# Performance work log

Hardware: AMD Instinct MI355X
Metric: run time of the kernel (lower is better)

## Reference

```python
import jax, jax.numpy as jnp
import numpy as np
from jax import lax

HEADS = 8
LN_EPS = 1e-5


def setup_inputs() -> dict:
    key = jax.random.key(0)
    k = jax.random.split(key, 8)
    B, C, H, W, r = 4, 64, 64, 64, 4
    T = H * W
    x = jax.random.normal(k[0], (B, C, H, W), dtype=jnp.float32)
    conv_w = jax.random.normal(k[1], (C, C, r, r), dtype=jnp.float32) * 0.02  # OIHW
    conv_b = jnp.zeros((C,), dtype=jnp.float32)
    ln_g = jnp.ones((C,), dtype=jnp.float32)
    ln_b = jnp.zeros((C,), dtype=jnp.float32)
    Wqkv = jax.random.normal(k[2], (C, 3 * C), dtype=jnp.float32) * 0.02  # to_qvk (no bias)
    W0 = jax.random.normal(k[3], (C, C), dtype=jnp.float32) * 0.02  # output proj (no bias)
    E = jax.random.normal(k[4], (T, T // 4), dtype=jnp.float32)  # Linformer proj (randn in torch fwd)
    return {"x": x, "conv_w": conv_w, "conv_b": conv_b, "ln_g": ln_g,
            "ln_b": ln_b, "Wqkv": Wqkv, "W0": W0, "E": E}


def _layernorm2d(y, g, b):
    # LayerNorm over channel dim of NCHW (torch: permute to NHWC, LN last dim)
    yt = y.transpose(0, 2, 3, 1)  # b h w c
    mu = yt.mean(-1, keepdims=True)
    var = ((yt - mu) ** 2).mean(-1, keepdims=True)
    yt = (yt - mu) * lax.rsqrt(var + LN_EPS) * g + b
    return yt.transpose(0, 3, 1, 2)


def reference(x, conv_w, conv_b, ln_g, ln_b, Wqkv, W0, E):
    B, C, H, W = x.shape
    T = H * W
    dh = C // HEADS
    r = conv_w.shape[-1]

    # reducer: conv(stride=r) + LayerNorm2d. NOTE: faithful to the torch module,
    # this result is computed but NEVER used by the output (dead code in source).
    red = lax.conv_general_dilated(x, conv_w, (r, r), 'VALID',
                                   dimension_numbers=('NCHW', 'OIHW', 'NCHW'))
    red = red + conv_b[None, :, None, None]
    _red = _layernorm2d(red, ln_g, ln_b)  # unused, matches source

    # tokens from full-resolution x: b c h w -> b (h w) c
    xf = x.reshape(B, C, T).transpose(0, 2, 1)  # [B,T,C]
    qkv = xf @ Wqkv  # [B,T,3C]
    # rearrange 'b t (d k h)' with k=3, h=HEADS -> composite order (d, k, h)
    qkv = qkv.reshape(B, T, dh, 3, HEADS)
    q = qkv[:, :, :, 0, :].transpose(0, 3, 1, 2)  # [B,h,T,d]
    kk = qkv[:, :, :, 1, :].transpose(0, 3, 1, 2)
    v = qkv[:, :, :, 2, :].transpose(0, 3, 1, 2)

    # Linformer low-rank projection of V and K: [B,h,T,d] x [T,k] -> [B,h,k,d]
    v = jnp.einsum('bhjd,jk->bhkd', v, E)
    kk = jnp.einsum('bhjd,jk->bhkd', kk, E)

    scale = dh ** -0.5
    scores = jnp.einsum('bhid,bhjd->bhij', q, kk) * scale  # [B,h,T,k]
    attn = jax.nn.softmax(scores, axis=-1)
    out = jnp.einsum('bhij,bhjd->bhid', attn, v)  # [B,h,T,d]

    out = out.transpose(0, 2, 1, 3).reshape(B, T, C)  # b h i d -> b i (h d)
    out = out @ W0  # [B,T,C]
    return out.transpose(0, 2, 1).reshape(B, C, H, W)
```

## Files before the change

kernel.cpp:

```cpp
#include <hip/hip_runtime.h>

#define T_DIM 4096
#define KD    1024
#define SCALE2 (0.35355339059327373f * 1.4426950408889634f)
#define XS2_PITCH 520
#define XP_PITCH 17
#define WK_PITCH 136
#define VC_H 648

extern "C" __device__ float __ocml_native_exp2_f32(float);

typedef __attribute__((ext_vector_type(8))) short bf16x8;
typedef __attribute__((ext_vector_type(4))) float f32x4;
typedef __attribute__((ext_vector_type(16))) float f32x16;

__device__ inline unsigned short f2bf(float f) {
  unsigned u = __float_as_uint(f);
  unsigned r = u + 0x7fffu + ((u >> 16) & 1u);
  return (unsigned short)(r >> 16);
}

__device__ inline unsigned cvt_pk_bf16(float a, float b) {
  unsigned ua = __float_as_uint(a); ua += 0x7fffu + ((ua >> 16) & 1u);
  unsigned ub = __float_as_uint(b); ub += 0x7fffu + ((ub >> 16) & 1u);
  return (ua >> 16) | (ub & 0xffff0000u);
}

__device__ inline bf16x8 mk8(unsigned a, unsigned b, unsigned c, unsigned d) {
  union { unsigned u[4]; bf16x8 v; } x;
  x.u[0] = a; x.u[1] = b; x.u[2] = c; x.u[3] = d; return x.v;
}

__global__ __launch_bounds__(1024) void k_front(const float* __restrict__ x,
                                                const float* __restrict__ E,
                                                const float* __restrict__ Wqkv,
                                                uint2* __restrict__ Kg,
                                                unsigned short* __restrict__ Vg,
                                                float* __restrict__ Q) {
  __shared__ __attribute__((aligned(16))) float SMEM[17408];
  __shared__ __attribute__((aligned(16))) float Wkvs[64 * WK_PITCH];
  __shared__ __attribute__((aligned(16))) float XPfull[64 * 33];
  unsigned short* xs = (unsigned short*)SMEM;
  float* XPs = SMEM;

  const int bid = blockIdx.x;
  const int tid = threadIdx.x;

  if (bid < 128) {
    const int kb2 = (bid & 7) + 8 * (bid >> 5);
    const int b   = (bid >> 3) & 3;
    const int k0  = kb2 * 32;
    const int lane = tid & 63, w = tid >> 6;
    const int li = lane & 15, lg = lane >> 4;

#pragma unroll
    for (int i = 0; i < 8; ++i) {
      const int idx = tid + i * 1024;
      const int c = idx >> 7, j = idx & 127;
      const int cg = j >> 3, d = j & 7;
      const int sel = (cg < 8) ? 1 : 2, h = cg & 7;
      Wkvs[c * WK_PITCH + j] = Wqkv[c * 192 + sel * 8 + h + d * 24];
    }

    const int tl  = (tid & 255) * 2;
    const int chp = tid >> 8;
    const int tloc = w * 32 + lg * 8;

    f32x4 acc[4][2] = {};
    for (int ct = 0; ct < 8; ++ct) {
      float ev0[8], ev1[8];
      const int tb = ct * 512 + tloc;
#pragma unroll
      for (int j = 0; j < 8; ++j) {
        ev0[j] = E[(size_t)(tb + j) * KD + k0 + li];
        ev1[j] = E[(size_t)(tb + j) * KD + k0 + 16 + li];
      }

      const float* xb = x + ((size_t)b * 64 + chp) * T_DIM + ct * 512 + tl;
#pragma unroll 4
      for (int it = 0; it < 16; ++it) {
        const int c = it * 4 + chp;
        float2 v = *(const float2*)(xb + (size_t)(it * 4) * T_DIM);
        *(unsigned*)(&xs[c * XS2_PITCH + tl]) = cvt_pk_bf16(v.x, v.y);
      }
      __syncthreads();

      bf16x8 bq0 = mk8(cvt_pk_bf16(ev0[0], ev0[1]), cvt_pk_bf16(ev0[2], ev0[3]),
                       cvt_pk_bf16(ev0[4], ev0[5]), cvt_pk_bf16(ev0[6], ev0[7]));
      bf16x8 bq1 = mk8(cvt_pk_bf16(ev1[0], ev1[1]), cvt_pk_bf16(ev1[2], ev1[3]),
                       cvt_pk_bf16(ev1[4], ev1[5]), cvt_pk_bf16(ev1[6], ev1[7]));
#pragma unroll
      for (int mt = 0; mt < 4; ++mt) {
        bf16x8 af8 = *(const bf16x8*)(&xs[(mt * 16 + li) * XS2_PITCH + tloc]);
        acc[mt][0] = __builtin_amdgcn_mfma_f32_16x16x32_bf16(af8, bq0, acc[mt][0], 0, 0, 0);
        acc[mt][1] = __builtin_amdgcn_mfma_f32_16x16x32_bf16(af8, bq1, acc[mt][1], 0, 0, 0);
      }
      __syncthreads();
    }

#pragma unroll
    for (int g = 0; g < 2; ++g) {
#pragma unroll
      for (int mt = 0; mt < 4; ++mt)
#pragma unroll
        for (int r = 0; r < 4; ++r)
          XPs[(w * 64 + mt * 16 + lg * 4 + r) * XP_PITCH + li] = acc[mt][g][r];
      __syncthreads();
      {
        const int c = tid >> 4, k = tid & 15;
        float s = 0.f;
#pragma unroll
        for (int wp = 0; wp < 16; ++wp) s += XPs[(wp * 64 + c) * XP_PITCH + k];
        XPfull[c * 33 + g * 16 + k] = s;
      }
      __syncthreads();
    }

    {
      const int k  = tid & 31;
      const int cg = (tid >> 5) & 15;
      const int dh = tid >> 9;
      float a4[4] = {0.f, 0.f, 0.f, 0.f};
#pragma unroll 8
      for (int c = 0; c < 64; ++c) {
        const float xv = XPfull[c * 33 + k];
        const float4 wv = *(const float4*)(&Wkvs[c * WK_PITCH + cg * 8 + dh * 4]);
        a4[0] += xv * wv.x; a4[1] += xv * wv.y;
        a4[2] += xv * wv.z; a4[3] += xv * wv.w;
      }
      const int h = cg & 7, bh = b * 8 + h, kk2 = k0 + k;
      if (cg < 8) {
        Kg[(size_t)bh * 2048 + kk2 * 2 + dh] =
            make_uint2(cvt_pk_bf16(a4[0] * SCALE2, a4[1] * SCALE2),
                       cvt_pk_bf16(a4[2] * SCALE2, a4[3] * SCALE2));
      } else {
#pragma unroll
        for (int d = 0; d < 4; ++d)
          Vg[(size_t)(bh * 8 + dh * 4 + d) * KD + kk2] = f2bf(a4[d]);
      }
    }
  } else {
    const int idx = bid - 128;
    const int g  = idx & 7;
    const int tt = (idx >> 3) & 3;
    const int b  = idx >> 5;
    const int t  = tt * 1024 + tid;
    const int col0 = g * 24;

    float acc[8];
#pragma unroll
    for (int j = 0; j < 8; ++j) acc[j] = 0.f;
    const float* xb = x + (size_t)b * 64 * T_DIM + t;
#pragma unroll 4
    for (int c = 0; c < 64; ++c) {
      float xv = xb[(size_t)c * T_DIM];
      const float* wr = Wqkv + c * 192 + col0;
#pragma unroll
      for (int h = 0; h < 8; ++h) acc[h] += xv * wr[h];
    }
#pragma unroll
    for (int h = 0; h < 8; ++h)
      Q[(((size_t)(b * 8 + h)) * 8 + g) * T_DIM + t] = acc[h];
  }
}

__global__ __launch_bounds__(512, 4) void k_attn(const float* __restrict__ Q,
                                                 const uint2* __restrict__ Kg,
                                                 const unsigned short* __restrict__ Vg,
                                                 const float* __restrict__ W0,
                                                 float* __restrict__ out) {
  __shared__ __attribute__((aligned(16))) unsigned short Kc[2][8 * 64 * 8];
  __shared__ __attribute__((aligned(16))) unsigned short Vc[2][8 * VC_H];
  __shared__ __attribute__((aligned(16))) float W0s[64 * 64];

  const int iy = blockIdx.x;
  const int b  = blockIdx.y;
  const int tid = threadIdx.x;
  const int w = tid >> 6;
  const int lane = tid & 63;
  const int icol = lane & 31, half = lane >> 5;
  const int i0 = iy * 32;
  const int bh = b * 8 + w;

#pragma unroll
  for (int i = 0; i < 8; ++i) W0s[tid + i * 512] = W0[tid + i * 512];

  {
    const int bu = tid >> 8, h = (tid >> 5) & 7, j2 = tid & 31;
    *(unsigned*)(&Vc[bu][h * VC_H + 8 * 72 + j2 * 2]) = 0x3F803F80u;
  }

  bf16x8 qf8 = {};
  if (lane < 32) {
    const float* qp = Q + (size_t)bh * 8 * T_DIM + i0 + icol;
    float q0 = qp[0],          q1 = qp[T_DIM],     q2 = qp[2 * T_DIM];
    float q3 = qp[3 * T_DIM],  q4 = qp[4 * T_DIM], q5 = qp[5 * T_DIM];
    float q6 = qp[6 * T_DIM],  q7 = qp[7 * T_DIM];
    qf8 = mk8(cvt_pk_bf16(q0, q1), cvt_pk_bf16(q2, q3),
              cvt_pk_bf16(q4, q5), cvt_pk_bf16(q6, q7));
  }

  const uint4* kg4    = (const uint4*)Kg + (size_t)b * 8192;
  const unsigned* vg2 = (const unsigned*)Vg + (size_t)b * 32768;

  {
    const int h = tid >> 6, j = tid & 63;
    *(uint4*)(&Kc[0][(h * 64 + j) * 8]) = kg4[h * 1024 + j];
#pragma unroll
    for (int i = 0; i < 4; ++i) {
      const int idx = tid + i * 512;
      const int hh = idx >> 8, d = (idx >> 5) & 7, j2 = idx & 31;
      *(unsigned*)(&Vc[0][hh * VC_H + d * 72 + j2 * 2]) = vg2[(hh * 8 + d) * 512 + j2];
    }
  }
  __syncthreads();

  f32x16 accO = {};
  int buf = 0;
  for (int jc = 0; jc < 16; ++jc) {
    uint4 kreg = {}; unsigned vreg[4] = {};
    if (jc < 15) {
      const int h = tid >> 6, j = tid & 63;
      kreg = kg4[h * 1024 + (jc + 1) * 64 + j];
#pragma unroll
      for (int i = 0; i < 4; ++i) {
        const int idx = tid + i * 512;
        const int hh = idx >> 8, d = (idx >> 5) & 7, j2 = idx & 31;
        vreg[i] = vg2[(hh * 8 + d) * 512 + (jc + 1) * 32 + j2];
      }
    }

#pragma unroll
    for (int sub = 0; sub < 2; ++sub) {
      const int jl = sub * 32;
      bf16x8 kf8 = {};
      if (lane < 32) kf8 = *(const bf16x8*)(&Kc[buf][(w * 64 + jl + lane) * 8]);
      f32x16 z = {};
      __builtin_amdgcn_s_setprio(1);
      f32x16 st = __builtin_amdgcn_mfma_f32_32x32x16_bf16(kf8, qf8, z, 0, 0, 0);
      __builtin_amdgcn_s_setprio(0);

      unsigned e0, e1, e2, e3, e4, e5, e6, e7;
      {
        float p0  = __ocml_native_exp2_f32(st[0]),  p1  = __ocml_native_exp2_f32(st[1]);
        float p2  = __ocml_native_exp2_f32(st[2]),  p3  = __ocml_native_exp2_f32(st[3]);
        float p4  = __ocml_native_exp2_f32(st[4]),  p5  = __ocml_native_exp2_f32(st[5]);
        float p6  = __ocml_native_exp2_f32(st[6]),  p7  = __ocml_native_exp2_f32(st[7]);
        float p8  = __ocml_native_exp2_f32(st[8]),  p9  = __ocml_native_exp2_f32(st[9]);
        float p10 = __ocml_native_exp2_f32(st[10]), p11 = __ocml_native_exp2_f32(st[11]);
        float p12 = __ocml_native_exp2_f32(st[12]), p13 = __ocml_native_exp2_f32(st[13]);
        float p14 = __ocml_native_exp2_f32(st[14]), p15 = __ocml_native_exp2_f32(st[15]);
        asm("v_cvt_pk_bf16_f32 %0, %1, %2" : "=v"(e0) : "v"(p0),  "v"(p1));
        asm("v_cvt_pk_bf16_f32 %0, %1, %2" : "=v"(e1) : "v"(p2),  "v"(p3));
        asm("v_cvt_pk_bf16_f32 %0, %1, %2" : "=v"(e2) : "v"(p4),  "v"(p5));
        asm("v_cvt_pk_bf16_f32 %0, %1, %2" : "=v"(e3) : "v"(p6),  "v"(p7));
        asm("v_cvt_pk_bf16_f32 %0, %1, %2" : "=v"(e4) : "v"(p8),  "v"(p9));
        asm("v_cvt_pk_bf16_f32 %0, %1, %2" : "=v"(e5) : "v"(p10), "v"(p11));
        asm("v_cvt_pk_bf16_f32 %0, %1, %2" : "=v"(e6) : "v"(p12), "v"(p13));
        asm("v_cvt_pk_bf16_f32 %0, %1, %2" : "=v"(e7) : "v"(p14), "v"(p15));
      }
      asm("v_permlane32_swap_b32 %0, %1" : "+v"(e0), "+v"(e2));
      asm("v_permlane32_swap_b32 %0, %1" : "+v"(e1), "+v"(e3));
      asm("v_permlane32_swap_b32 %0, %1" : "+v"(e4), "+v"(e6));
      asm("v_permlane32_swap_b32 %0, %1" : "+v"(e5), "+v"(e7));

      bf16x8 va0 = {}, va1 = {};
      if (icol < 9) {
        const unsigned short* vp = &Vc[buf][w * VC_H + icol * 72 + jl + half * 8];
        va0 = *(const bf16x8*)(vp);
        va1 = *(const bf16x8*)(vp + 16);
      }
      __builtin_amdgcn_s_setprio(1);
      accO = __builtin_amdgcn_mfma_f32_32x32x16_bf16(va0, mk8(e0, e1, e2, e3), accO, 0, 0, 0);
      accO = __builtin_amdgcn_mfma_f32_32x32x16_bf16(va1, mk8(e4, e5, e6, e7), accO, 0, 0, 0);
      __builtin_amdgcn_s_setprio(0);
    }

    if (jc < 15) {
      const int h = tid >> 6, j = tid & 63;
      *(uint4*)(&Kc[buf ^ 1][(h * 64 + j) * 8]) = kreg;
#pragma unroll
      for (int i = 0; i < 4; ++i) {
        const int idx = tid + i * 512;
        const int hh = idx >> 8, d = (idx >> 5) & 7, j2 = idx & 31;
        *(unsigned*)(&Vc[buf ^ 1][hh * VC_H + d * 72 + j2 * 2]) = vreg[i];
      }
    }
    __syncthreads();
    buf ^= 1;
  }

  float* Os = (float*)Kc;
  {
    float inv = 1.0f / __shfl(accO[4], icol);
    if (lane < 32 || half) {
      float4 o = make_float4(accO[0] * inv, accO[1] * inv,
                             accO[2] * inv, accO[3] * inv);
      *(float2*)(&Os[icol * 66 + w * 8 + half * 4])     = make_float2(o.x, o.y);
      *(float2*)(&Os[icol * 66 + w * 8 + half * 4 + 2]) = make_float2(o.z, o.w);
    }
  }
  __syncthreads();

  {
    const int tok = tid & 31, cq = tid >> 5;
    float o4[4] = {0.f, 0.f, 0.f, 0.f};
#pragma unroll 8
    for (int hd = 0; hd < 64; ++hd) {
      const float ov = Os[tok * 66 + hd];
      const float4 wv = *(const float4*)(&W0s[hd * 64 + cq * 4]);
      o4[0] += ov * wv.x; o4[1] += ov * wv.y;
      o4[2] += ov * wv.z; o4[3] += ov * wv.w;
    }
#pragma unroll
    for (int cc = 0; cc < 4; ++cc)
      out[((size_t)b * 64 + cq * 4 + cc) * T_DIM + i0 + tok] = o4[cc];
  }
}

extern "C" void kernel_launch(void* const* d_in, const int* in_sizes, int n_in,
                              void* d_out, int out_size, void* d_ws, size_t ws_size,
                              hipStream_t stream) {
  const float* x    = (const float*)d_in[0];
  const float* Wqkv = (const float*)d_in[5];
  const float* W0   = (const float*)d_in[6];
  const float* E    = (const float*)d_in[7];
  float* out = (float*)d_out;

  float* Q           = (float*)d_ws;
  uint2* Kg          = (uint2*)(Q + 1048576);
  unsigned short* Vg = (unsigned short*)(Kg + 65536);

  k_front <<<dim3(256),    1024, 0, stream>>>(x, E, Wqkv, Kg, Vg, Q);
  k_attn  <<<dim3(128, 4), 512,  0, stream>>>(Q, Kg, Vg, W0, out);
}
```

Baseline: 137.1 us.

## Add prep kernel converting E (transposed) and x to bf16 before front GEMM

A new k_prep kernel transposes E into a k-major bf16 buffer and converts x to bf16 in workspace. k_front then loads its MFMA operands directly from these bf16 buffers as 16-byte vector reads, dropping the LDS staging and the per-tile barriers. In exchange it adds a kernel launch and an extra pass that writes and rereads about 8MB of E in bf16. E is recomputed on every call, so this is not a caching hack.

```diff
diff --git a/kernel.cpp b/kernel.cpp
--- a/kernel.cpp
+++ b/kernel.cpp
@@ -3,7 +3,6 @@
 #define T_DIM 4096
 #define KD    1024
 #define SCALE2 (0.35355339059327373f * 1.4426950408889634f)
-#define XS2_PITCH 520
 #define XP_PITCH 17
 #define WK_PITCH 136
 #define VC_H 648
@@ -31,17 +30,49 @@
   x.u[0] = a; x.u[1] = b; x.u[2] = c; x.u[3] = d; return x.v;
 }
 
-__global__ __launch_bounds__(1024) void k_front(const float* __restrict__ x,
-                                                const float* __restrict__ E,
+__global__ __launch_bounds__(256) void k_prep(const float* __restrict__ E,
+                                              const float* __restrict__ x,
+                                              unsigned short* __restrict__ Et,
+                                              unsigned short* __restrict__ xbf) {
+  const int bid = blockIdx.x;
+  const int tid = threadIdx.x;
+
+  if (bid < 256) {
+    const int kk = (bid & 15) * 64 + (tid & 63);
+    const int t0 = (((bid >> 4) << 2) + (tid >> 6)) * 64;
+    const float* ep = E + (size_t)t0 * KD + kk;
+    unsigned short* eo = Et + (size_t)kk * T_DIM + t0;
+#pragma unroll
+    for (int i = 0; i < 8; ++i) {
+      float v[8];
+#pragma unroll
+      for (int j = 0; j < 8; ++j)
+        v[j] = ep[(size_t)(i * 8 + j) * KD];
+      *(bf16x8*)(eo + i * 8) = mk8(cvt_pk_bf16(v[0], v[1]), cvt_pk_bf16(v[2], v[3]),
+                                   cvt_pk_bf16(v[4], v[5]), cvt_pk_bf16(v[6], v[7]));
+    }
+  } else {
+    const int idx = bid - 256;
+    const float4* xp = (const float4*)x + (size_t)idx * 4096;
+    uint2* xo = (uint2*)xbf + (size_t)idx * 4096;
+#pragma unroll 4
+    for (int i = 0; i < 16; ++i) {
+      float4 v = xp[tid + i * 256];
+      xo[tid + i * 256] = make_uint2(cvt_pk_bf16(v.x, v.y), cvt_pk_bf16(v.z, v.w));
+    }
+  }
+}
+
+__global__ __launch_bounds__(1024) void k_front(const unsigned short* __restrict__ xbf,
+                                                const float* __restrict__ x,
+                                                const unsigned short* __restrict__ Et,
                                                 const float* __restrict__ Wqkv,
                                                 uint2* __restrict__ Kg,
                                                 unsigned short* __restrict__ Vg,
                                                 float* __restrict__ Q) {
-  __shared__ __attribute__((aligned(16))) float SMEM[17408];
+  __shared__ __attribute__((aligned(16))) float XPs[16 * 64 * XP_PITCH];
   __shared__ __attribute__((aligned(16))) float Wkvs[64 * WK_PITCH];
   __shared__ __attribute__((aligned(16))) float XPfull[64 * 33];
-  unsigned short* xs = (unsigned short*)SMEM;
-  float* XPs = SMEM;
 
   const int bid = blockIdx.x;
   const int tid = threadIdx.x;
@@ -62,41 +93,24 @@
       Wkvs[c * WK_PITCH + j] = Wqkv[c * 192 + sel * 8 + h + d * 24];
     }
 
-    const int tl  = (tid & 255) * 2;
-    const int chp = tid >> 8;
-    const int tloc = w * 32 + lg * 8;
+    const unsigned short* xr  = xbf + (size_t)b * 64 * T_DIM;
+    const unsigned short* e0p = Et + (size_t)(k0 + li) * T_DIM;
+    const unsigned short* e1p = Et + (size_t)(k0 + 16 + li) * T_DIM;
 
     f32x4 acc[4][2] = {};
-    for (int ct = 0; ct < 8; ++ct) {
-      float ev0[8], ev1[8];
-      const int tb = ct * 512 + tloc;
-#pragma unroll
-      for (int j = 0; j < 8; ++j) {
-        ev0[j] = E[(size_t)(tb + j) * KD + k0 + li];
-        ev1[j] = E[(size_t)(tb + j) * KD + k0 + 16 + li];
-      }
-
-      const float* xb = x + ((size_t)b * 64 + chp) * T_DIM + ct * 512 + tl;
-#pragma unroll 4
-      for (int it = 0; it < 16; ++it) {
-        const int c = it * 4 + chp;
-        float2 v = *(const float2*)(xb + (size_t)(it * 4) * T_DIM);
-        *(unsigned*)(&xs[c * XS2_PITCH + tl]) = cvt_pk_bf16(v.x, v.y);
-      }
-      __syncthreads();
-
-      bf16x8 bq0 = mk8(cvt_pk_bf16(ev0[0], ev0[1]), cvt_pk_bf16(ev0[2], ev0[3]),
-                       cvt_pk_bf16(ev0[4], ev0[5]), cvt_pk_bf16(ev0[6], ev0[7]));
-      bf16x8 bq1 = mk8(cvt_pk_bf16(ev1[0], ev1[1]), cvt_pk_bf16(ev1[2], ev1[3]),
-                       cvt_pk_bf16(ev1[4], ev1[5]), cvt_pk_bf16(ev1[6], ev1[7]));
+#pragma unroll
+    for (int s = 0; s < 8; ++s) {
+      const int tb = (s * 16 + w) * 32 + lg * 8;
+      bf16x8 bq0 = *(const bf16x8*)(e0p + tb);
+      bf16x8 bq1 = *(const bf16x8*)(e1p + tb);
 #pragma unroll
       for (int mt = 0; mt < 4; ++mt) {
-        bf16x8 af8 = *(const bf16x8*)(&xs[(mt * 16 + li) * XS2_PITCH + tloc]);
-        acc[mt][0] = __builtin_amdgcn_mfma_f32_16x16x32_bf16(af8, bq0, acc[mt][0], 0, 0, 0);
-        acc[mt][1] = __builtin_amdgcn_mfma_f32_16x16x32_bf16(af8, bq1, acc[mt][1], 0, 0, 0);
-      }
-      __syncthreads();
-    }
+        bf16x8 af = *(const bf16x8*)(xr + (size_t)(mt * 16 + li) * T_DIM + tb);
+        acc[mt][0] = __builtin_amdgcn_mfma_f32_16x16x32_bf16(af, bq0, acc[mt][0], 0, 0, 0);
+        acc[mt][1] = __builtin_amdgcn_mfma_f32_16x16x32_bf16(af, bq1, acc[mt][1], 0, 0, 0);
+      }
+    }
+    __syncthreads();
 
 #pragma unroll
     for (int g = 0; g < 2; ++g) {
@@ -327,10 +341,13 @@
   const float* E    = (const float*)d_in[7];
   float* out = (float*)d_out;
 
-  float* Q           = (float*)d_ws;
-  uint2* Kg          = (uint2*)(Q + 1048576);
-  unsigned short* Vg = (unsigned short*)(Kg + 65536);
-
-  k_front <<<dim3(256),    1024, 0, stream>>>(x, E, Wqkv, Kg, Vg, Q);
+  float* Q            = (float*)d_ws;
+  uint2* Kg           = (uint2*)(Q + 1048576);
+  unsigned short* Vg  = (unsigned short*)(Kg + 65536);
+  unsigned short* Et  = Vg + 262144;
+  unsigned short* xbf = Et + 4194304;
+
+  k_prep  <<<dim3(320),    256,  0, stream>>>(E, x, Et, xbf);
+  k_front <<<dim3(256),    1024, 0, stream>>>(xbf, x, Et, Wqkv, Kg, Vg, Q);
   k_attn  <<<dim3(128, 4), 512,  0, stream>>>(Q, Kg, Vg, W0, out);
 }
```

Result: no change. 139.5 us (+1.7%).
